# Kernel optimization log

Measured on AMD Instinct MI355X. Metric: run time of the kernel, lower is better.

Reference implementation:

```python
import jax, jax.numpy as jnp
import numpy as np

B, T, C, H = 4, 2048, 1024, 16
HS = C // H  # head size = 64

def setup_inputs() -> dict:
    key = jax.random.key(0)
    ks = jax.random.split(key, 3)
    x = jax.random.normal(ks[0], (B, T, C), dtype=jnp.float32)
    w_attn = jax.random.normal(ks[1], (C, 3 * C), dtype=jnp.float32) * (1.0 / np.sqrt(C))
    b_attn = jnp.zeros((3 * C,), dtype=jnp.float32)
    w_proj = jax.random.normal(ks[2], (C, C), dtype=jnp.float32) * (1.0 / np.sqrt(C))
    b_proj = jnp.zeros((C,), dtype=jnp.float32)
    return {"x": x, "w_attn": w_attn, "b_attn": b_attn, "w_proj": w_proj, "b_proj": b_proj}

def reference(x, w_attn, b_attn, w_proj, b_proj):
    b, t, c = x.shape
    qkv = x @ w_attn + b_attn                       # [B,T,3C]
    q, k, v = jnp.split(qkv, 3, axis=2)             # each [B,T,C]
    # [B,T,C] -> [B,H,T,HS]
    q = q.reshape(b, t, H, HS).transpose(0, 2, 1, 3)
    k = k.reshape(b, t, H, HS).transpose(0, 2, 1, 3)
    v = v.reshape(b, t, H, HS).transpose(0, 2, 1, 3)
    scale = 1.0 / np.sqrt(HS)
    att = jnp.einsum('bhqd,bhkd->bhqk', q, k) * scale   # [B,H,T,T]
    causal = jnp.tril(jnp.ones((t, t), dtype=bool))
    att = jnp.where(causal[None, None, :, :], att, -jnp.inf)
    att = jax.nn.softmax(att, axis=-1)
    y = jnp.einsum('bhqk,bhkd->bhqd', att, v)           # [B,H,T,HS]
    y = y.transpose(0, 2, 1, 3).reshape(b, t, c)        # [B,T,C]
    return y @ w_proj + b_proj
```

## Files before the change

### kernel.cpp

```cpp
#include <hip/hip_runtime.h>
#include <hip/hip_bf16.h>

#define B_ 4
#define T_ 2048
#define C_ 1024
#define H_ 16
#define HS_ 64
#define M_ (B_*T_)

typedef __bf16 bf16_t;
typedef bf16_t bf16x8 __attribute__((ext_vector_type(8)));
typedef float f32x4 __attribute__((ext_vector_type(4)));
typedef unsigned short ushort_t;

__device__ __forceinline__ unsigned short f2bf(float f) {
    __hip_bfloat16 h = __float2bfloat16(f);
    return __builtin_bit_cast(unsigned short, h);
}

__device__ __forceinline__ void glds16(const void* g, void* l) {
    __builtin_amdgcn_global_load_lds((const __attribute__((address_space(1))) void*)g,
                                     (__attribute__((address_space(3))) void*)l, 16, 0, 0);
}

__launch_bounds__(256)
__global__ void cvt_x(const float* __restrict__ in, ushort_t* __restrict__ out) {
    int i = blockIdx.x * 256 + threadIdx.x;
    const float4* p = (const float4*)in;
    float4 a = p[i * 2], b = p[i * 2 + 1];
    ushort4 o0, o1;
    o0.x = f2bf(a.x); o0.y = f2bf(a.y); o0.z = f2bf(a.z); o0.w = f2bf(a.w);
    o1.x = f2bf(b.x); o1.y = f2bf(b.y); o1.z = f2bf(b.z); o1.w = f2bf(b.w);
    *(ushort4*)&out[i * 8] = o0;
    *(ushort4*)&out[i * 8 + 4] = o1;
}

__launch_bounds__(256)
__global__ void transpose_cvt(const float* __restrict__ w, ushort_t* __restrict__ wT,
                              int K, int N) {
    __shared__ ushort_t Ts[64][72];
    const int n0 = blockIdx.x * 64, k0 = blockIdx.y * 64;
    const int t = threadIdx.x, r = t >> 2, cq = t & 3;
    #pragma unroll
    for (int j = 0; j < 4; j++) {
        float4 v = *(const float4*)&w[(size_t)(k0 + r) * N + n0 + cq * 16 + j * 4];
        ushort4 o;
        o.x = f2bf(v.x); o.y = f2bf(v.y); o.z = f2bf(v.z); o.w = f2bf(v.w);
        *(ushort4*)&Ts[r][cq * 16 + j * 4] = o;
    }
    __syncthreads();
    #pragma unroll
    for (int j = 0; j < 4; j++) {
        ushort4 o;
        o.x = Ts[cq * 16 + j * 4 + 0][r];
        o.y = Ts[cq * 16 + j * 4 + 1][r];
        o.z = Ts[cq * 16 + j * 4 + 2][r];
        o.w = Ts[cq * 16 + j * 4 + 3][r];
        *(ushort4*)&wT[(size_t)(n0 + r) * K + k0 + cq * 16 + j * 4] = o;
    }
}

__launch_bounds__(256)
__global__ void qkv_gemm(const ushort_t* __restrict__ xb, const ushort_t* __restrict__ wT,
                         const float* __restrict__ bias,
                         ushort_t* __restrict__ qw, ushort_t* __restrict__ kw,
                         ushort_t* __restrict__ vt) {
    const int K = C_;
    __shared__ ushort_t As[128 * 32];
    __shared__ ushort_t Bs[128 * 32];
    const int tid = threadIdx.x, lane = tid & 63, wid = tid >> 6;
    const int cl = lane & 15, gl = lane >> 4;
    const int waveM = wid >> 1, waveN = wid & 1;
    const int m0 = blockIdx.y * 128, n0 = blockIdx.x * 128;
    const int srow = tid >> 2, scq = tid & 3;

    f32x4 acc[4][4];
    #pragma unroll
    for (int mf = 0; mf < 4; mf++)
        #pragma unroll
        for (int nf = 0; nf < 4; nf++) acc[mf][nf] = (f32x4)0.0f;

    for (int kk = 0; kk < K; kk += 32) {
        #pragma unroll
        for (int i = 0; i < 2; i++) {
            int c = tid + i * 256;
            int row = srow + i * 64;
            glds16(&xb[(size_t)(m0 + row) * K + kk + scq * 8], &As[(size_t)c * 8]);
            glds16(&wT[(size_t)(n0 + row) * K + kk + scq * 8], &Bs[(size_t)c * 8]);
        }
        __syncthreads();
        bf16x8 a[4], b[4];
        #pragma unroll
        for (int mf = 0; mf < 4; mf++)
            a[mf] = *(bf16x8*)&As[(waveM * 64 + mf * 16 + cl) * 32 + gl * 8];
        #pragma unroll
        for (int nf = 0; nf < 4; nf++)
            b[nf] = *(bf16x8*)&Bs[(waveN * 64 + nf * 16 + cl) * 32 + gl * 8];
        #pragma unroll
        for (int mf = 0; mf < 4; mf++)
            #pragma unroll
            for (int nf = 0; nf < 4; nf++)
                acc[mf][nf] = __builtin_amdgcn_mfma_f32_16x16x32_bf16(a[mf], b[nf], acc[mf][nf], 0, 0, 0);
        __syncthreads();
    }
    const int secb = n0 >> 10;
    #pragma unroll
    for (int mf = 0; mf < 4; mf++)
        #pragma unroll
        for (int nf = 0; nf < 4; nf++)
            #pragma unroll
            for (int r = 0; r < 4; r++) {
                int rg = m0 + waveM * 64 + mf * 16 + 4 * gl + r;
                int cg = n0 + waveN * 64 + nf * 16 + cl;
                float val = acc[mf][nf][r] + bias[cg];
                int cc = cg & 1023;
                int h = cc >> 6, hs = cc & 63;
                int bb = rg >> 11, tq = rg & 2047;
                if (secb == 0)
                    qw[(((size_t)(bb * H_ + h)) * T_ + tq) * HS_ + hs] = f2bf(val);
                else if (secb == 1)
                    kw[(((size_t)(bb * H_ + h)) * T_ + tq) * HS_ + hs] = f2bf(val);
                else
                    vt[(((size_t)(bb * H_ + h)) * HS_ + hs) * T_ + tq] = f2bf(val);
            }
}

__launch_bounds__(256, 2)
__global__ void attn_mfma(const ushort_t* __restrict__ qw,
                          const ushort_t* __restrict__ kw,
                          const ushort_t* __restrict__ vt,
                          ushort_t* __restrict__ yw) {
    __shared__ ushort_t Ks[64][72];
    __shared__ ushort_t Vts[64][72];
    __shared__ ushort_t Ps[4][32][72];
    const int tid = threadIdx.x, lane = tid & 63, wid = tid >> 6;
    const int cl = lane & 15, gl = lane >> 4;
    const int qp = blockIdx.x;
    const int bh = blockIdx.y;
    const size_t base = (size_t)bh * T_ * HS_;
    const int bq = bh >> 4, h = bh & 15;
    const int srow = tid >> 3, scq = tid & 7;

    for (int half = 0; half < 2; half++) {
        const int qt = half ? (15 - qp) : qp;
        const int q0 = qt * 128 + wid * 32;
        const int ntiles = 2 * qt + 2;

        bf16x8 qf[2][2];
        #pragma unroll
        for (int qm = 0; qm < 2; qm++)
            #pragma unroll
            for (int kh = 0; kh < 2; kh++)
                qf[qm][kh] = *(const bf16x8*)&qw[base + (size_t)(q0 + qm * 16 + cl) * HS_ + kh * 32 + 8 * gl];

        f32x4 o_acc[2][4];
        #pragma unroll
        for (int qm = 0; qm < 2; qm++)
            #pragma unroll
            for (int dn = 0; dn < 4; dn++) o_acc[qm][dn] = (f32x4)0.0f;
        float m_[2][4], l_[2][4];
        #pragma unroll
        for (int qm = 0; qm < 2; qm++)
            #pragma unroll
            for (int r = 0; r < 4; r++) { m_[qm][r] = -INFINITY; l_[qm][r] = 0.f; }

        bf16x8 kpre[2], vpre[2], knew[2], vnew[2];
        #pragma unroll
        for (int i = 0; i < 2; i++) {
            int row = srow + i * 32;
            kpre[i] = *(const bf16x8*)&kw[base + (size_t)row * HS_ + scq * 8];
            vpre[i] = *(const bf16x8*)&vt[base + (size_t)row * T_ + scq * 8];
        }

        for (int kt = 0; kt < ntiles; kt++) {
            __syncthreads();
            if (kt + 1 < ntiles) {
                #pragma unroll
                for (int i = 0; i < 2; i++) {
                    int row = srow + i * 32;
                    knew[i] = *(const bf16x8*)&kw[base + (size_t)((kt + 1) * 64 + row) * HS_ + scq * 8];
                    vnew[i] = *(const bf16x8*)&vt[base + (size_t)row * T_ + (kt + 1) * 64 + scq * 8];
                }
            }
            #pragma unroll
            for (int i = 0; i < 2; i++) {
                int row = srow + i * 32;
                *(bf16x8*)&Ks[row][scq * 8] = kpre[i];
                *(bf16x8*)&Vts[row][scq * 8] = vpre[i];
            }
            __syncthreads();

            bf16x8 kf[4][2];
            #pragma unroll
            for (int kn = 0; kn < 4; kn++)
                #pragma unroll
                for (int kh = 0; kh < 2; kh++)
                    kf[kn][kh] = *(bf16x8*)&Ks[kn * 16 + cl][kh * 32 + 8 * gl];
            f32x4 s[2][4];
            #pragma unroll
            for (int qm = 0; qm < 2; qm++)
                #pragma unroll
                for (int kn = 0; kn < 4; kn++) {
                    f32x4 t0 = (f32x4)0.0f;
                    t0 = __builtin_amdgcn_mfma_f32_16x16x32_bf16(qf[qm][0], kf[kn][0], t0, 0, 0, 0);
                    s[qm][kn] = __builtin_amdgcn_mfma_f32_16x16x32_bf16(qf[qm][1], kf[kn][1], t0, 0, 0, 0);
                }

            float alpha[2][4];
            #pragma unroll
            for (int qm = 0; qm < 2; qm++) {
                #pragma unroll
                for (int kn = 0; kn < 4; kn++)
                    #pragma unroll
                    for (int r = 0; r < 4; r++) {
                        int kv = kt * 64 + kn * 16 + cl;
                        int qg = q0 + qm * 16 + 4 * gl + r;
                        float v = s[qm][kn][r] * 0.125f;
                        s[qm][kn][r] = (kv <= qg) ? v : -INFINITY;
                    }
                #pragma unroll
                for (int r = 0; r < 4; r++) {
                    float mx = fmaxf(fmaxf(s[qm][0][r], s[qm][1][r]),
                                     fmaxf(s[qm][2][r], s[qm][3][r]));
                    #pragma unroll
                    for (int off = 8; off >= 1; off >>= 1) mx = fmaxf(mx, __shfl_xor(mx, off));
                    float nm = fmaxf(m_[qm][r], mx);
                    float al = __expf(m_[qm][r] - nm);
                    m_[qm][r] = nm;
                    alpha[qm][r] = al;
                    float ps = 0.f;
                    #pragma unroll
                    for (int kn = 0; kn < 4; kn++) {
                        float p = __expf(s[qm][kn][r] - nm);
                        s[qm][kn][r] = p;
                        ps += p;
                    }
                    l_[qm][r] = l_[qm][r] * al + ps;
                }
            }

            #pragma unroll
            for (int qm = 0; qm < 2; qm++)
                #pragma unroll
                for (int kn = 0; kn < 4; kn++)
                    #pragma unroll
                    for (int r = 0; r < 4; r++)
                        Ps[wid][qm * 16 + 4 * gl + r][kn * 16 + cl] = f2bf(s[qm][kn][r]);

            #pragma unroll
            for (int qm = 0; qm < 2; qm++)
                #pragma unroll
                for (int dn = 0; dn < 4; dn++)
                    #pragma unroll
                    for (int r = 0; r < 4; r++)
                        o_acc[qm][dn][r] *= alpha[qm][r];

            bf16x8 pf[2][2], vf[4][2];
            #pragma unroll
            for (int qm = 0; qm < 2; qm++)
                #pragma unroll
                for (int ks = 0; ks < 2; ks++)
                    pf[qm][ks] = *(bf16x8*)&Ps[wid][qm * 16 + cl][ks * 32 + 8 * gl];
            #pragma unroll
            for (int dn = 0; dn < 4; dn++)
                #pragma unroll
                for (int ks = 0; ks < 2; ks++)
                    vf[dn][ks] = *(bf16x8*)&Vts[dn * 16 + cl][ks * 32 + 8 * gl];
            #pragma unroll
            for (int qm = 0; qm < 2; qm++)
                #pragma unroll
                for (int dn = 0; dn < 4; dn++)
                    #pragma unroll
                    for (int ks = 0; ks < 2; ks++)
                        o_acc[qm][dn] = __builtin_amdgcn_mfma_f32_16x16x32_bf16(
                            pf[qm][ks], vf[dn][ks], o_acc[qm][dn], 0, 0, 0);

            #pragma unroll
            for (int i = 0; i < 2; i++) { kpre[i] = knew[i]; vpre[i] = vnew[i]; }
        }

        #pragma unroll
        for (int qm = 0; qm < 2; qm++)
            #pragma unroll
            for (int r = 0; r < 4; r++) {
                float l = l_[qm][r];
                #pragma unroll
                for (int off = 8; off >= 1; off >>= 1) l += __shfl_xor(l, off);
                l_[qm][r] = 1.0f / l;
            }
        #pragma unroll
        for (int qm = 0; qm < 2; qm++)
            #pragma unroll
            for (int dn = 0; dn < 4; dn++)
                #pragma unroll
                for (int r = 0; r < 4; r++) {
                    int qg = q0 + qm * 16 + 4 * gl + r;
                    int d = dn * 16 + cl;
                    yw[((size_t)(bq * T_ + qg)) * C_ + h * HS_ + d] =
                        f2bf(o_acc[qm][dn][r] * l_[qm][r]);
                }
    }
}

__launch_bounds__(256)
__global__ void proj_gemm(const ushort_t* __restrict__ y, const ushort_t* __restrict__ wT,
                          const float* __restrict__ bias, float* __restrict__ out) {
    const int K = C_, N = C_;
    __shared__ ushort_t As[128 * 32];
    __shared__ ushort_t Bs[128 * 32];
    const int tid = threadIdx.x, lane = tid & 63, wid = tid >> 6;
    const int cl = lane & 15, gl = lane >> 4;
    const int waveM = wid >> 1, waveN = wid & 1;
    const int m0 = blockIdx.y * 128, n0 = blockIdx.x * 128;
    const int srow = tid >> 2, scq = tid & 3;

    f32x4 acc[4][4];
    #pragma unroll
    for (int mf = 0; mf < 4; mf++)
        #pragma unroll
        for (int nf = 0; nf < 4; nf++) acc[mf][nf] = (f32x4)0.0f;

    for (int kk = 0; kk < K; kk += 32) {
        #pragma unroll
        for (int i = 0; i < 2; i++) {
            int c = tid + i * 256;
            int row = srow + i * 64;
            glds16(&y[(size_t)(m0 + row) * K + kk + scq * 8], &As[(size_t)c * 8]);
            glds16(&wT[(size_t)(n0 + row) * K + kk + scq * 8], &Bs[(size_t)c * 8]);
        }
        __syncthreads();
        bf16x8 a[4], b[4];
        #pragma unroll
        for (int mf = 0; mf < 4; mf++)
            a[mf] = *(bf16x8*)&As[(waveM * 64 + mf * 16 + cl) * 32 + gl * 8];
        #pragma unroll
        for (int nf = 0; nf < 4; nf++)
            b[nf] = *(bf16x8*)&Bs[(waveN * 64 + nf * 16 + cl) * 32 + gl * 8];
        #pragma unroll
        for (int mf = 0; mf < 4; mf++)
            #pragma unroll
            for (int nf = 0; nf < 4; nf++)
                acc[mf][nf] = __builtin_amdgcn_mfma_f32_16x16x32_bf16(a[mf], b[nf], acc[mf][nf], 0, 0, 0);
        __syncthreads();
    }
    #pragma unroll
    for (int mf = 0; mf < 4; mf++)
        #pragma unroll
        for (int nf = 0; nf < 4; nf++)
            #pragma unroll
            for (int r = 0; r < 4; r++) {
                int rg = m0 + waveM * 64 + mf * 16 + 4 * gl + r;
                int cg = n0 + waveN * 64 + nf * 16 + cl;
                out[(size_t)rg * N + cg] = acc[mf][nf][r] + bias[cg];
            }
}

extern "C" void kernel_launch(void* const* d_in, const int* in_sizes, int n_in,
                              void* d_out, int out_size, void* d_ws, size_t ws_size,
                              hipStream_t stream) {
    const float* x      = (const float*)d_in[0];
    const float* w_attn = (const float*)d_in[1];
    const float* b_attn = (const float*)d_in[2];
    const float* w_proj = (const float*)d_in[3];
    const float* b_proj = (const float*)d_in[4];
    float* out = (float*)d_out;

    const size_t E = (size_t)M_ * C_;
    ushort_t* qw  = (ushort_t*)d_ws;
    ushort_t* kw  = qw + E;
    ushort_t* vt  = kw + E;
    ushort_t* xy  = vt + E;
    ushort_t* wat = xy + E;
    ushort_t* wpt = vt;

    cvt_x<<<dim3(4096), 256, 0, stream>>>(x, xy);
    transpose_cvt<<<dim3(48, 16), 256, 0, stream>>>(w_attn, wat, C_, 3 * C_);
    qkv_gemm<<<dim3(24, 64), 256, 0, stream>>>(xy, wat, b_attn, qw, kw, vt);
    attn_mfma<<<dim3(8, 64), 256, 0, stream>>>(qw, kw, vt, xy);
    transpose_cvt<<<dim3(16, 16), 256, 0, stream>>>(w_proj, wpt, C_, C_);
    proj_gemm<<<dim3(8, 64), 256, 0, stream>>>(xy, wpt, b_proj, out);
}
```

Before: 332.3 us.

## Restructure attention to 8 waves of 16 queries with transposed scores and causal skip

The attention kernel now runs 512 threads per block, each wave owning 16 query rows, and computes S^T (K as A operand) so each lane holds one query's scores. Per-wave causal skipping drops fully masked key tiles, and masking is applied only on diagonal tiles. The softmax scale and log2(e) are folded into Q in the QKV GEMM epilogue so exp2f can be used, and P is packed to bf16 with v_cvt_pk_bf16_f32. Per-row reductions use fewer shuffles. The cost is more shuffles to broadcast alpha and 1/l per output row, plus smaller per-wave MFMA reuse of K/V fragments.

```diff
diff --git a/kernel.cpp b/kernel.cpp
--- a/kernel.cpp
+++ b/kernel.cpp
@@ -7,6 +7,7 @@
 #define H_ 16
 #define HS_ 64
 #define M_ (B_*T_)
+#define QSCALE 0.18033688011112042f
 
 typedef __bf16 bf16_t;
 typedef bf16_t bf16x8 __attribute__((ext_vector_type(8)));
@@ -117,7 +118,7 @@
                 int h = cc >> 6, hs = cc & 63;
                 int bb = rg >> 11, tq = rg & 2047;
                 if (secb == 0)
-                    qw[(((size_t)(bb * H_ + h)) * T_ + tq) * HS_ + hs] = f2bf(val);
+                    qw[(((size_t)(bb * H_ + h)) * T_ + tq) * HS_ + hs] = f2bf(val * QSCALE);
                 else if (secb == 1)
                     kw[(((size_t)(bb * H_ + h)) * T_ + tq) * HS_ + hs] = f2bf(val);
                 else
@@ -125,14 +126,14 @@
             }
 }
 
-__launch_bounds__(256, 2)
+__launch_bounds__(512, 4)
 __global__ void attn_mfma(const ushort_t* __restrict__ qw,
                           const ushort_t* __restrict__ kw,
                           const ushort_t* __restrict__ vt,
                           ushort_t* __restrict__ yw) {
     __shared__ ushort_t Ks[64][72];
     __shared__ ushort_t Vts[64][72];
-    __shared__ ushort_t Ps[4][32][72];
+    __shared__ ushort_t Ps[8][16][72];
     const int tid = threadIdx.x, lane = tid & 63, wid = tid >> 6;
     const int cl = lane & 15, gl = lane >> 4;
     const int qp = blockIdx.x;
@@ -143,162 +144,118 @@
 
     for (int half = 0; half < 2; half++) {
         const int qt = half ? (15 - qp) : qp;
-        const int q0 = qt * 128 + wid * 32;
+        const int q0 = qt * 128 + wid * 16;
         const int ntiles = 2 * qt + 2;
 
-        bf16x8 qf[2][2];
-        #pragma unroll
-        for (int qm = 0; qm < 2; qm++)
-            #pragma unroll
-            for (int kh = 0; kh < 2; kh++)
-                qf[qm][kh] = *(const bf16x8*)&qw[base + (size_t)(q0 + qm * 16 + cl) * HS_ + kh * 32 + 8 * gl];
-
-        f32x4 o_acc[2][4];
-        #pragma unroll
-        for (int qm = 0; qm < 2; qm++)
-            #pragma unroll
-            for (int dn = 0; dn < 4; dn++) o_acc[qm][dn] = (f32x4)0.0f;
-        float m_[2][4], l_[2][4];
-        #pragma unroll
-        for (int qm = 0; qm < 2; qm++)
-            #pragma unroll
-            for (int r = 0; r < 4; r++) { m_[qm][r] = -INFINITY; l_[qm][r] = 0.f; }
-
-        bf16x8 kpre[2], vpre[2], knew[2], vnew[2];
-        #pragma unroll
-        for (int i = 0; i < 2; i++) {
-            int row = srow + i * 32;
-            kpre[i] = *(const bf16x8*)&kw[base + (size_t)row * HS_ + scq * 8];
-            vpre[i] = *(const bf16x8*)&vt[base + (size_t)row * T_ + scq * 8];
-        }
+        bf16x8 qf[2];
+        #pragma unroll
+        for (int kh = 0; kh < 2; kh++)
+            qf[kh] = *(const bf16x8*)&qw[base + (size_t)(q0 + cl) * HS_ + kh * 32 + 8 * gl];
+
+        f32x4 o_acc[4];
+        #pragma unroll
+        for (int dn = 0; dn < 4; dn++) o_acc[dn] = (f32x4)0.0f;
+        float m_ = -INFINITY, l_ = 0.f;
+
+        bf16x8 kpre, vpre, knew, vnew;
+        kpre = *(const bf16x8*)&kw[base + (size_t)srow * HS_ + scq * 8];
+        vpre = *(const bf16x8*)&vt[base + (size_t)srow * T_ + scq * 8];
 
         for (int kt = 0; kt < ntiles; kt++) {
             __syncthreads();
             if (kt + 1 < ntiles) {
-                #pragma unroll
-                for (int i = 0; i < 2; i++) {
-                    int row = srow + i * 32;
-                    knew[i] = *(const bf16x8*)&kw[base + (size_t)((kt + 1) * 64 + row) * HS_ + scq * 8];
-                    vnew[i] = *(const bf16x8*)&vt[base + (size_t)row * T_ + (kt + 1) * 64 + scq * 8];
-                }
-            }
-            #pragma unroll
-            for (int i = 0; i < 2; i++) {
-                int row = srow + i * 32;
-                *(bf16x8*)&Ks[row][scq * 8] = kpre[i];
-                *(bf16x8*)&Vts[row][scq * 8] = vpre[i];
-            }
+                knew = *(const bf16x8*)&kw[base + (size_t)((kt + 1) * 64 + srow) * HS_ + scq * 8];
+                vnew = *(const bf16x8*)&vt[base + (size_t)srow * T_ + (kt + 1) * 64 + scq * 8];
+            }
+            *(bf16x8*)&Ks[srow][scq * 8] = kpre;
+            *(bf16x8*)&Vts[srow][scq * 8] = vpre;
             __syncthreads();
 
-            bf16x8 kf[4][2];
-            #pragma unroll
-            for (int kn = 0; kn < 4; kn++)
-                #pragma unroll
-                for (int kh = 0; kh < 2; kh++)
-                    kf[kn][kh] = *(bf16x8*)&Ks[kn * 16 + cl][kh * 32 + 8 * gl];
-            f32x4 s[2][4];
-            #pragma unroll
-            for (int qm = 0; qm < 2; qm++)
+            if (kt * 64 <= q0 + 15) {
+                const bool full = (kt * 64 + 63 <= q0);
+
+                f32x4 st[4];
                 #pragma unroll
                 for (int kn = 0; kn < 4; kn++) {
+                    bf16x8 kf0 = *(bf16x8*)&Ks[kn * 16 + cl][8 * gl];
+                    bf16x8 kf1 = *(bf16x8*)&Ks[kn * 16 + cl][32 + 8 * gl];
                     f32x4 t0 = (f32x4)0.0f;
-                    t0 = __builtin_amdgcn_mfma_f32_16x16x32_bf16(qf[qm][0], kf[kn][0], t0, 0, 0, 0);
-                    s[qm][kn] = __builtin_amdgcn_mfma_f32_16x16x32_bf16(qf[qm][1], kf[kn][1], t0, 0, 0, 0);
-                }
-
-            float alpha[2][4];
-            #pragma unroll
-            for (int qm = 0; qm < 2; qm++) {
+                    t0 = __builtin_amdgcn_mfma_f32_16x16x32_bf16(kf0, qf[0], t0, 0, 0, 0);
+                    st[kn] = __builtin_amdgcn_mfma_f32_16x16x32_bf16(kf1, qf[1], t0, 0, 0, 0);
+                }
+                if (!full) {
+                    const int qg = q0 + cl;
+                    #pragma unroll
+                    for (int kn = 0; kn < 4; kn++)
+                        #pragma unroll
+                        for (int r = 0; r < 4; r++) {
+                            int kv = kt * 64 + kn * 16 + 4 * gl + r;
+                            if (kv > qg) st[kn][r] = -INFINITY;
+                        }
+                }
+
+                float mx = st[0][0];
                 #pragma unroll
                 for (int kn = 0; kn < 4; kn++)
                     #pragma unroll
-                    for (int r = 0; r < 4; r++) {
-                        int kv = kt * 64 + kn * 16 + cl;
-                        int qg = q0 + qm * 16 + 4 * gl + r;
-                        float v = s[qm][kn][r] * 0.125f;
-                        s[qm][kn][r] = (kv <= qg) ? v : -INFINITY;
-                    }
+                    for (int r = 0; r < 4; r++) mx = fmaxf(mx, st[kn][r]);
+                mx = fmaxf(mx, __shfl_xor(mx, 16));
+                mx = fmaxf(mx, __shfl_xor(mx, 32));
+                float nm = fmaxf(m_, mx);
+                float nmu = (nm > -INFINITY) ? nm : 0.0f;
+                float al = exp2f(m_ - nmu);
+                m_ = nm;
+
+                float ps = 0.f;
+                #pragma unroll
+                for (int kn = 0; kn < 4; kn++) {
+                    float p0 = exp2f(st[kn][0] - nmu);
+                    float p1 = exp2f(st[kn][1] - nmu);
+                    float p2 = exp2f(st[kn][2] - nmu);
+                    float p3 = exp2f(st[kn][3] - nmu);
+                    ps += (p0 + p1) + (p2 + p3);
+                    unsigned lo, hi;
+                    asm("v_cvt_pk_bf16_f32 %0, %1, %2" : "=v"(lo) : "v"(p0), "v"(p1));
+                    asm("v_cvt_pk_bf16_f32 %0, %1, %2" : "=v"(hi) : "v"(p2), "v"(p3));
+                    uint2 wv; wv.x = lo; wv.y = hi;
+                    *(uint2*)&Ps[wid][cl][kn * 16 + 4 * gl] = wv;
+                }
+                l_ = l_ * al + ps;
+
                 #pragma unroll
                 for (int r = 0; r < 4; r++) {
-                    float mx = fmaxf(fmaxf(s[qm][0][r], s[qm][1][r]),
-                                     fmaxf(s[qm][2][r], s[qm][3][r]));
+                    float ag = __shfl(al, 4 * gl + r);
                     #pragma unroll
-                    for (int off = 8; off >= 1; off >>= 1) mx = fmaxf(mx, __shfl_xor(mx, off));
-                    float nm = fmaxf(m_[qm][r], mx);
-                    float al = __expf(m_[qm][r] - nm);
-                    m_[qm][r] = nm;
-                    alpha[qm][r] = al;
-                    float ps = 0.f;
-                    #pragma unroll
-                    for (int kn = 0; kn < 4; kn++) {
-                        float p = __expf(s[qm][kn][r] - nm);
-                        s[qm][kn][r] = p;
-                        ps += p;
-                    }
-                    l_[qm][r] = l_[qm][r] * al + ps;
-                }
-            }
-
-            #pragma unroll
-            for (int qm = 0; qm < 2; qm++)
-                #pragma unroll
-                for (int kn = 0; kn < 4; kn++)
-                    #pragma unroll
-                    for (int r = 0; r < 4; r++)
-                        Ps[wid][qm * 16 + 4 * gl + r][kn * 16 + cl] = f2bf(s[qm][kn][r]);
-
-            #pragma unroll
-            for (int qm = 0; qm < 2; qm++)
-                #pragma unroll
-                for (int dn = 0; dn < 4; dn++)
-                    #pragma unroll
-                    for (int r = 0; r < 4; r++)
-                        o_acc[qm][dn][r] *= alpha[qm][r];
-
-            bf16x8 pf[2][2], vf[4][2];
-            #pragma unroll
-            for (int qm = 0; qm < 2; qm++)
-                #pragma unroll
-                for (int ks = 0; ks < 2; ks++)
-                    pf[qm][ks] = *(bf16x8*)&Ps[wid][qm * 16 + cl][ks * 32 + 8 * gl];
-            #pragma unroll
-            for (int dn = 0; dn < 4; dn++)
-                #pragma unroll
-                for (int ks = 0; ks < 2; ks++)
-                    vf[dn][ks] = *(bf16x8*)&Vts[dn * 16 + cl][ks * 32 + 8 * gl];
-            #pragma unroll
-            for (int qm = 0; qm < 2; qm++)
-                #pragma unroll
-                for (int dn = 0; dn < 4; dn++)
-                    #pragma unroll
-                    for (int ks = 0; ks < 2; ks++)
-                        o_acc[qm][dn] = __builtin_amdgcn_mfma_f32_16x16x32_bf16(
-                            pf[qm][ks], vf[dn][ks], o_acc[qm][dn], 0, 0, 0);
-
-            #pragma unroll
-            for (int i = 0; i < 2; i++) { kpre[i] = knew[i]; vpre[i] = vnew[i]; }
+                    for (int dn = 0; dn < 4; dn++) o_acc[dn][r] *= ag;
+                }
+
+                bf16x8 pf0 = *(bf16x8*)&Ps[wid][cl][8 * gl];
+                bf16x8 pf1 = *(bf16x8*)&Ps[wid][cl][32 + 8 * gl];
+                #pragma unroll
+                for (int dn = 0; dn < 4; dn++) {
+                    bf16x8 vf0 = *(bf16x8*)&Vts[dn * 16 + cl][8 * gl];
+                    bf16x8 vf1 = *(bf16x8*)&Vts[dn * 16 + cl][32 + 8 * gl];
+                    o_acc[dn] = __builtin_amdgcn_mfma_f32_16x16x32_bf16(pf0, vf0, o_acc[dn], 0, 0, 0);
+                    o_acc[dn] = __builtin_amdgcn_mfma_f32_16x16x32_bf16(pf1, vf1, o_acc[dn], 0, 0, 0);
+                }
+            }
+            if (kt + 1 < ntiles) { kpre = knew; vpre = vnew; }
         }
 
-        #pragma unroll
-        for (int qm = 0; qm < 2; qm++)
-            #pragma unroll
-            for (int r = 0; r < 4; r++) {
-                float l = l_[qm][r];
-                #pragma unroll
-                for (int off = 8; off >= 1; off >>= 1) l += __shfl_xor(l, off);
-                l_[qm][r] = 1.0f / l;
-            }
-        #pragma unroll
-        for (int qm = 0; qm < 2; qm++)
-            #pragma unroll
-            for (int dn = 0; dn < 4; dn++)
-                #pragma unroll
-                for (int r = 0; r < 4; r++) {
-                    int qg = q0 + qm * 16 + 4 * gl + r;
-                    int d = dn * 16 + cl;
-                    yw[((size_t)(bq * T_ + qg)) * C_ + h * HS_ + d] =
-                        f2bf(o_acc[qm][dn][r] * l_[qm][r]);
-                }
+        float ls = l_;
+        ls += __shfl_xor(ls, 16);
+        ls += __shfl_xor(ls, 32);
+        float linv = 1.0f / ls;
+        #pragma unroll
+        for (int r = 0; r < 4; r++) {
+            float lr = __shfl(linv, 4 * gl + r);
+            int qg = q0 + 4 * gl + r;
+            #pragma unroll
+            for (int dn = 0; dn < 4; dn++) {
+                int d = dn * 16 + cl;
+                yw[((size_t)(bq * T_ + qg)) * C_ + h * HS_ + d] = f2bf(o_acc[dn][r] * lr);
+            }
+        }
     }
 }
 
@@ -376,7 +333,7 @@
     cvt_x<<<dim3(4096), 256, 0, stream>>>(x, xy);
     transpose_cvt<<<dim3(48, 16), 256, 0, stream>>>(w_attn, wat, C_, 3 * C_);
     qkv_gemm<<<dim3(24, 64), 256, 0, stream>>>(xy, wat, b_attn, qw, kw, vt);
-    attn_mfma<<<dim3(8, 64), 256, 0, stream>>>(qw, kw, vt, xy);
+    attn_mfma<<<dim3(8, 64), 512, 0, stream>>>(qw, kw, vt, xy);
     transpose_cvt<<<dim3(16, 16), 256, 0, stream>>>(w_proj, wpt, C_, C_);
     proj_gemm<<<dim3(8, 64), 256, 0, stream>>>(xy, wpt, b_proj, out);
 }
```

Result: faster. 295.8 us (-11.0%).
